# Performance work log

Measured on AMD Instinct MI355X. Metric: run time of the kernel, lower is better.

The kernel has to match this reference:

```python
import jax, jax.numpy as jnp
import numpy as np
from jax import lax

T, B, D, H, C = 2048, 64, 128, 256, 5

def setup_inputs() -> dict:
    key = jax.random.key(0)
    k = jax.random.split(key, 7)
    s = 1.0 / np.sqrt(H)  # pytorch nn.RNN init scale
    return {
        "inputs": jax.random.normal(k[0], (T, B, D), dtype=jnp.float32),
        "W_ih": jax.random.uniform(k[1], (H, D), jnp.float32, -s, s),
        "W_hh": jax.random.uniform(k[2], (H, H), jnp.float32, -s, s),
        "b_ih": jax.random.uniform(k[3], (H,), jnp.float32, -s, s),
        "b_hh": jax.random.uniform(k[4], (H,), jnp.float32, -s, s),
        "W_fc": jax.random.uniform(k[5], (C, H), jnp.float32, -s, s),
        "b_fc": jax.random.uniform(k[6], (C,), jnp.float32, -s, s),
    }

def reference(inputs, W_ih, W_hh, b_ih, b_hh, W_fc, b_fc):
    # Precompute input projections for all timesteps: (T, B, H)
    x_proj = jnp.einsum('tbd,hd->tbh', inputs, W_ih) + b_ih + b_hh

    def step(h, xp):
        # h_t = tanh(W_ih x_t + b_ih + W_hh h_{t-1} + b_hh)
        h_new = jnp.tanh(xp + h @ W_hh.T)
        return h_new, None  # per-step outputs unused by the module head

    h0 = jnp.zeros((inputs.shape[1], W_hh.shape[0]), dtype=inputs.dtype)
    h_last, _ = lax.scan(step, h0, x_proj)

    logits = h_last @ W_fc.T + b_fc  # (B, 5)
    return jax.nn.log_softmax(logits, axis=1)
```

## Files before the change

### kernel.cpp

```cpp
#include <hip/hip_runtime.h>


#define T_DIM 2048
#define B_DIM 64
#define D_DIM 128
#define H_DIM 256
#define C_DIM 5

using floatx4 = __attribute__((ext_vector_type(4))) float;
using shortx8 = __attribute__((ext_vector_type(8))) short;

#define W_SCALE 2032.0f
#define H_SCALE 127.0f
#define INV_SCALE (1.0f / (2032.0f * 127.0f))

__device__ __forceinline__ short f2bf(float f) {
  unsigned int u = __float_as_uint(f);
  unsigned int r = (u + 0x7FFFu + ((u >> 16) & 1u)) >> 16;
  return (short)r;
}

__device__ __forceinline__ int sdot4(unsigned int a, unsigned int b, int c) {
#if __has_builtin(__builtin_amdgcn_sdot4)
  return __builtin_amdgcn_sdot4((int)a, (int)b, c, false);
#else
  int r = c;
  #pragma unroll
  for (int k = 0; k < 4; ++k)
    r += (int)(signed char)(a >> (8 * k)) * (int)(signed char)(b >> (8 * k));
  return r;
#endif
}

template<int CTRL>
__device__ __forceinline__ int dpp_movi(int x) {
  return __builtin_amdgcn_update_dpp(0, x, CTRL, 0xF, 0xF, true);
}

__device__ __forceinline__ void barrier_lds_only() {
  asm volatile("s_waitcnt lgkmcnt(0)\n\ts_barrier" ::: "memory");
}

#define TS_PER_BLOCK 2
__global__ __launch_bounds__(256) void xp_kernel(
    const float* __restrict__ x,
    const float* __restrict__ W_ih,
    const float* __restrict__ b_ih,
    const float* __restrict__ b_hh,
    _Float16* __restrict__ xp,
    int cnt)
{
  __shared__ __align__(16) short wlds[32768];
  const int tid = threadIdx.x;
  {
    const int group = tid >> 2;
    const int sub = tid & 3;
    const int kf = group & 3;
    const int k0 = kf * 32 + sub * 8;
    #pragma unroll
    for (int i = 0; i < 16; ++i) {
      const int n = (group >> 2) * 16 + i;
      const float* src = W_ih + n * D_DIM + k0;
      float4 p0 = *(const float4*)(src);
      float4 p1 = *(const float4*)(src + 4);
      shortx8 v;
      v[0]=f2bf(p0.x); v[1]=f2bf(p0.y); v[2]=f2bf(p0.z); v[3]=f2bf(p0.w);
      v[4]=f2bf(p1.x); v[5]=f2bf(p1.y); v[6]=f2bf(p1.z); v[7]=f2bf(p1.w);
      *(shortx8*)&wlds[(group * 64 + sub * 16 + i) * 8] = v;
    }
  }
  __syncthreads();

  const int wv   = tid >> 6;
  const int lane = tid & 63;
  const int col  = lane & 15;
  const int quad = lane >> 4;

  float bias[16];
  #pragma unroll
  for (int nt = 0; nt < 16; ++nt)
    bias[nt] = b_ih[nt * 16 + col] + b_hh[nt * 16 + col];

  for (int tl = 0; tl < TS_PER_BLOCK; ++tl) {
    const int t = blockIdx.x * TS_PER_BLOCK + tl;
    if (t >= cnt) break;
    const long m0 = (long)t * 64 + wv * 16;

    shortx8 af[4];
    const float* arow = x + (m0 + col) * D_DIM + quad * 8;
    #pragma unroll
    for (int kf = 0; kf < 4; ++kf) {
      float4 p0 = *(const float4*)(arow + kf * 32);
      float4 p1 = *(const float4*)(arow + kf * 32 + 4);
      shortx8 v;
      v[0]=f2bf(p0.x); v[1]=f2bf(p0.y); v[2]=f2bf(p0.z); v[3]=f2bf(p0.w);
      v[4]=f2bf(p1.x); v[5]=f2bf(p1.y); v[6]=f2bf(p1.z); v[7]=f2bf(p1.w);
      af[kf] = v;
    }

    #pragma unroll
    for (int nt = 0; nt < 16; ++nt) {
      floatx4 acc = {0.f, 0.f, 0.f, 0.f};
      #pragma unroll
      for (int kf = 0; kf < 4; ++kf) {
        shortx8 bfrag = *(const shortx8*)&wlds[((nt * 4 + kf) * 64 + lane) * 8];
        acc = __builtin_amdgcn_mfma_f32_16x16x32_bf16(af[kf], bfrag, acc, 0, 0, 0);
      }
      const int n = nt * 16 + col;
      #pragma unroll
      for (int r = 0; r < 4; ++r) {
        const long m = m0 + quad * 4 + r;
        xp[m * H_DIM + n] = (_Float16)(acc[r] + bias[nt]);
      }
    }
  }
}

__global__ __launch_bounds__(256)
__attribute__((amdgpu_waves_per_eu(1, 1)))
void scan_kernel(
    const _Float16* __restrict__ xp,
    const float* __restrict__ W_hh,
    const float* __restrict__ W_fc,
    const float* __restrict__ b_fc,
    float* __restrict__ h_state,
    float* __restrict__ out,
    int cnt, int first, int last)
{
  __shared__ __align__(16) signed char hbuf[2][256];
  __shared__ float hfin[H_DIM];
  __shared__ float scratch[192];
  const int b   = blockIdx.x;
  const int tid = threadIdx.x;
  const int g   = tid >> 2;
  const int c   = tid & 3;

  unsigned int wq[4][16];
  const float* wbase = W_hh + (g * 4) * H_DIM + c * 64;
  #pragma unroll
  for (int r = 0; r < 4; ++r)
    #pragma unroll
    for (int i = 0; i < 16; ++i) {
      float4 f = *(const float4*)(wbase + r * H_DIM + i * 4);
      unsigned int q0 = (unsigned int)(int)rintf(f.x * W_SCALE) & 0xFFu;
      unsigned int q1 = (unsigned int)(int)rintf(f.y * W_SCALE) & 0xFFu;
      unsigned int q2 = (unsigned int)(int)rintf(f.z * W_SCALE) & 0xFFu;
      unsigned int q3 = (unsigned int)(int)rintf(f.w * W_SCALE) & 0xFFu;
      wq[r][i] = q0 | (q1 << 8) | (q2 << 16) | (q3 << 24);
    }
  #pragma unroll
  for (int r = 0; r < 4; ++r)
    #pragma unroll
    for (int i = 0; i < 16; ++i)
      asm volatile("" : "+v"(wq[r][i]));

  const int row_w = tid;
  {
    float h0 = first ? 0.f : h_state[b * H_DIM + row_w];
    hbuf[0][row_w] = (signed char)(int)rintf(h0 * H_SCALE);
  }
  __syncthreads();

  const size_t BH = (size_t)B_DIM * H_DIM;
  const _Float16* xpp = xp + (size_t)b * H_DIM + row_w;
  float hnlast = 0.f;

  auto step_body = [&](int bufsel, _Float16 xin) -> void {
    const signed char* hb = hbuf[bufsel] + c * 64;
    uint4 u0 = *(const uint4*)(hb);
    uint4 u1 = *(const uint4*)(hb + 16);
    uint4 u2 = *(const uint4*)(hb + 32);
    uint4 u3 = *(const uint4*)(hb + 48);
    const unsigned int hv[16] = {u0.x, u0.y, u0.z, u0.w, u1.x, u1.y, u1.z, u1.w,
                                 u2.x, u2.y, u2.z, u2.w, u3.x, u3.y, u3.z, u3.w};
    int a0 = 0, a1 = 0, a2 = 0, a3 = 0;
    #pragma unroll
    for (int i = 0; i < 16; ++i) {
      a0 = sdot4(wq[0][i], hv[i], a0);
      a1 = sdot4(wq[1][i], hv[i], a1);
      a2 = sdot4(wq[2][i], hv[i], a2);
      a3 = sdot4(wq[3][i], hv[i], a3);
    }
    int k01 = (c & 1) ? a1 : a0;
    int s01 = (c & 1) ? a0 : a1;
    int m0  = k01 + dpp_movi<0xB1>(s01);
    int k23 = (c & 1) ? a3 : a2;
    int s23 = (c & 1) ? a2 : a3;
    int m1  = k23 + dpp_movi<0xB1>(s23);
    int kk = (c & 2) ? m1 : m0;
    int sn = (c & 2) ? m0 : m1;
    int vi = kk + dpp_movi<0x4E>(sn);

    float p = (float)vi * INV_SCALE + (float)xin;
    float e   = __expf(2.f * p);
    float hqf = 127.f - __fdividef(254.f, e + 1.f);
    hnlast = hqf;
    hbuf[bufsel ^ 1][row_w] = (signed char)(int)rintf(hqf);
    barrier_lds_only();
  };

  if ((cnt & 1) == 0 && cnt >= 2) {
    const _Float16* p = xpp;
    _Float16 x0 = p[0];
    _Float16 x1 = p[BH];
    int s = 0;
    for (; s + 2 < cnt; s += 2) {
      step_body(0, x0); x0 = p[2 * BH];
      step_body(1, x1); x1 = p[3 * BH];
      p += 2 * BH;
    }
    step_body(0, x0);
    step_body(1, x1);
  } else {
    for (int s = 0; s < cnt; ++s)
      step_body(s & 1, xpp[(size_t)s * BH]);
  }

  {
    const float hT = hnlast * (1.0f / 127.0f);
    h_state[b * H_DIM + row_w] = hT;
    hfin[row_w] = hT;
  }

  if (last) {
    __syncthreads();
    if (tid < 160) {
      const int c5 = tid >> 5, i = tid & 31;
      float pp = 0.f;
      #pragma unroll
      for (int jj = 0; jj < 8; ++jj) {
        const int j = i * 8 + jj;
        pp += W_fc[c5 * H_DIM + j] * hfin[j];
      }
      scratch[tid] = pp;
    }
    __syncthreads();
    if (tid < C_DIM) {
      float l = b_fc[tid];
      for (int i = 0; i < 32; ++i) l += scratch[tid * 32 + i];
      scratch[160 + tid] = l;
    }
    __syncthreads();
    if (tid == 0) {
      float mx = scratch[160];
      for (int i = 1; i < C_DIM; ++i) mx = fmaxf(mx, scratch[160 + i]);
      float se = 0.f;
      for (int i = 0; i < C_DIM; ++i) se += __expf(scratch[160 + i] - mx);
      const float lse = mx + __logf(se);
      for (int i = 0; i < C_DIM; ++i) out[b * C_DIM + i] = scratch[160 + i] - lse;
    }
  }
}

extern "C" void kernel_launch(void* const* d_in, const int* in_sizes, int n_in,
                              void* d_out, int out_size, void* d_ws, size_t ws_size,
                              hipStream_t stream) {
  (void)in_sizes; (void)n_in; (void)out_size;
  const float* x    = (const float*)d_in[0];
  const float* W_ih = (const float*)d_in[1];
  const float* W_hh = (const float*)d_in[2];
  const float* b_ih = (const float*)d_in[3];
  const float* b_hh = (const float*)d_in[4];
  const float* W_fc = (const float*)d_in[5];
  const float* b_fc = (const float*)d_in[6];
  float* out = (float*)d_out;

  char* ws = (char*)d_ws;
  float* h_state = (float*)ws;
  _Float16* xp = (_Float16*)(ws + 65536);
  const size_t avail = ws_size > 65536 ? ws_size - 65536 : 0;
  long Tc = (long)(avail / ((size_t)B_DIM * H_DIM * sizeof(_Float16)));
  if (Tc > T_DIM) Tc = T_DIM;
  if (Tc < 1) Tc = 1;

  for (long t0 = 0; t0 < T_DIM; t0 += Tc) {
    const long cnt = (T_DIM - t0 < Tc) ? (T_DIM - t0) : Tc;
    const unsigned xpb = (unsigned)((cnt + TS_PER_BLOCK - 1) / TS_PER_BLOCK);
    xp_kernel<<<dim3(xpb), dim3(256), 0, stream>>>(
        x + t0 * B_DIM * D_DIM, W_ih, b_ih, b_hh, xp, (int)cnt);
    scan_kernel<<<dim3(B_DIM), dim3(256), 0, stream>>>(
        xp, W_hh, W_fc, b_fc, h_state, out,
        (int)cnt, t0 == 0 ? 1 : 0, (t0 + cnt == T_DIM) ? 1 : 0);
  }
}
```

Baseline: 739.6 us.

## Keep W_ih fragments in registers and compute transposed xp tiles with vector stores

The input-projection kernel no longer stages W_ih in LDS. Each wave holds its 64-row slice of W_ih as bf16 MFMA A-fragments in registers and streams x rows as the B operand, so each output lane gets four consecutive hidden units. That lets the kernel write xp as 4-wide half vectors instead of scattered scalar stores. Timesteps per block rise from 2 to 4 to spread the register weight load. The cost is higher register pressure and reloading x per wave, and the scan kernel, which dominates runtime, is unchanged.

```diff
diff --git a/kernel.cpp b/kernel.cpp
--- a/kernel.cpp
+++ b/kernel.cpp
@@ -9,6 +9,7 @@
 
 using floatx4 = __attribute__((ext_vector_type(4))) float;
 using shortx8 = __attribute__((ext_vector_type(8))) short;
+using half4v  = __attribute__((ext_vector_type(4))) _Float16;
 
 #define W_SCALE 2032.0f
 #define H_SCALE 127.0f
@@ -41,7 +42,7 @@
   asm volatile("s_waitcnt lgkmcnt(0)\n\ts_barrier" ::: "memory");
 }
 
-#define TS_PER_BLOCK 2
+#define TS_PER_BLOCK 4
 __global__ __launch_bounds__(256) void xp_kernel(
     const float* __restrict__ x,
     const float* __restrict__ W_ih,
@@ -50,67 +51,64 @@
     _Float16* __restrict__ xp,
     int cnt)
 {
-  __shared__ __align__(16) short wlds[32768];
-  const int tid = threadIdx.x;
-  {
-    const int group = tid >> 2;
-    const int sub = tid & 3;
-    const int kf = group & 3;
-    const int k0 = kf * 32 + sub * 8;
-    #pragma unroll
-    for (int i = 0; i < 16; ++i) {
-      const int n = (group >> 2) * 16 + i;
-      const float* src = W_ih + n * D_DIM + k0;
-      float4 p0 = *(const float4*)(src);
-      float4 p1 = *(const float4*)(src + 4);
-      shortx8 v;
-      v[0]=f2bf(p0.x); v[1]=f2bf(p0.y); v[2]=f2bf(p0.z); v[3]=f2bf(p0.w);
-      v[4]=f2bf(p1.x); v[5]=f2bf(p1.y); v[6]=f2bf(p1.z); v[7]=f2bf(p1.w);
-      *(shortx8*)&wlds[(group * 64 + sub * 16 + i) * 8] = v;
-    }
-  }
-  __syncthreads();
-
+  const int tid  = threadIdx.x;
   const int wv   = tid >> 6;
   const int lane = tid & 63;
   const int col  = lane & 15;
   const int quad = lane >> 4;
 
-  float bias[16];
-  #pragma unroll
-  for (int nt = 0; nt < 16; ++nt)
-    bias[nt] = b_ih[nt * 16 + col] + b_hh[nt * 16 + col];
+  shortx8 af[4][4];
+  #pragma unroll
+  for (int mt = 0; mt < 4; ++mt) {
+    const float* wrow = W_ih + (wv * 64 + mt * 16 + col) * D_DIM + quad * 8;
+    #pragma unroll
+    for (int kf = 0; kf < 4; ++kf) {
+      float4 p0 = *(const float4*)(wrow + kf * 32);
+      float4 p1 = *(const float4*)(wrow + kf * 32 + 4);
+      shortx8 v;
+      v[0]=f2bf(p0.x); v[1]=f2bf(p0.y); v[2]=f2bf(p0.z); v[3]=f2bf(p0.w);
+      v[4]=f2bf(p1.x); v[5]=f2bf(p1.y); v[6]=f2bf(p1.z); v[7]=f2bf(p1.w);
+      af[mt][kf] = v;
+    }
+  }
+  float bias[4][4];
+  #pragma unroll
+  for (int mt = 0; mt < 4; ++mt)
+    #pragma unroll
+    for (int r = 0; r < 4; ++r) {
+      const int h = wv * 64 + mt * 16 + quad * 4 + r;
+      bias[mt][r] = b_ih[h] + b_hh[h];
+    }
 
   for (int tl = 0; tl < TS_PER_BLOCK; ++tl) {
     const int t = blockIdx.x * TS_PER_BLOCK + tl;
     if (t >= cnt) break;
-    const long m0 = (long)t * 64 + wv * 16;
-
-    shortx8 af[4];
-    const float* arow = x + (m0 + col) * D_DIM + quad * 8;
-    #pragma unroll
-    for (int kf = 0; kf < 4; ++kf) {
-      float4 p0 = *(const float4*)(arow + kf * 32);
-      float4 p1 = *(const float4*)(arow + kf * 32 + 4);
-      shortx8 v;
-      v[0]=f2bf(p0.x); v[1]=f2bf(p0.y); v[2]=f2bf(p0.z); v[3]=f2bf(p0.w);
-      v[4]=f2bf(p1.x); v[5]=f2bf(p1.y); v[6]=f2bf(p1.z); v[7]=f2bf(p1.w);
-      af[kf] = v;
-    }
-
-    #pragma unroll
-    for (int nt = 0; nt < 16; ++nt) {
-      floatx4 acc = {0.f, 0.f, 0.f, 0.f};
+    #pragma unroll
+    for (int nt = 0; nt < 4; ++nt) {
+      const float* xrow = x + ((long)t * 64 + nt * 16 + col) * D_DIM + quad * 8;
+      floatx4 acc[4] = {{0.f,0.f,0.f,0.f},{0.f,0.f,0.f,0.f},
+                        {0.f,0.f,0.f,0.f},{0.f,0.f,0.f,0.f}};
       #pragma unroll
       for (int kf = 0; kf < 4; ++kf) {
-        shortx8 bfrag = *(const shortx8*)&wlds[((nt * 4 + kf) * 64 + lane) * 8];
-        acc = __builtin_amdgcn_mfma_f32_16x16x32_bf16(af[kf], bfrag, acc, 0, 0, 0);
+        float4 p0 = *(const float4*)(xrow + kf * 32);
+        float4 p1 = *(const float4*)(xrow + kf * 32 + 4);
+        shortx8 bf;
+        bf[0]=f2bf(p0.x); bf[1]=f2bf(p0.y); bf[2]=f2bf(p0.z); bf[3]=f2bf(p0.w);
+        bf[4]=f2bf(p1.x); bf[5]=f2bf(p1.y); bf[6]=f2bf(p1.z); bf[7]=f2bf(p1.w);
+        #pragma unroll
+        for (int mt = 0; mt < 4; ++mt)
+          acc[mt] = __builtin_amdgcn_mfma_f32_16x16x32_bf16(af[mt][kf], bf, acc[mt], 0, 0, 0);
       }
-      const int n = nt * 16 + col;
+      _Float16* obase = xp + ((size_t)t * 64 + nt * 16 + col) * H_DIM
+                           + wv * 64 + quad * 4;
       #pragma unroll
-      for (int r = 0; r < 4; ++r) {
-        const long m = m0 + quad * 4 + r;
-        xp[m * H_DIM + n] = (_Float16)(acc[r] + bias[nt]);
+      for (int mt = 0; mt < 4; ++mt) {
+        half4v o;
+        o[0] = (_Float16)(acc[mt][0] + bias[mt][0]);
+        o[1] = (_Float16)(acc[mt][1] + bias[mt][1]);
+        o[2] = (_Float16)(acc[mt][2] + bias[mt][2]);
+        o[3] = (_Float16)(acc[mt][3] + bias[mt][3]);
+        *(half4v*)(obase + mt * 16) = o;
       }
     }
   }
```

Result: slower. 769.0 us (+4.0%).
